# Performance work log

Measured on AMD Instinct MI355X. Metric: run time of the kernel, lower is better.

Reference implementation:

```python
import jax, jax.numpy as jnp
import numpy as np

NUM_HEADS, NUM_KV_HEADS, HEAD_DIM, HIDDEN = 8, 1, 256, 2048
B, S = 1, 4096

def setup_inputs() -> dict:
    key = jax.random.key(0)
    ks = jax.random.split(key, 6)
    sd = 1.0 / np.sqrt(HIDDEN)
    x = jax.random.normal(ks[0], (B, S, HIDDEN), dtype=jnp.float32)
    wq = jax.random.normal(ks[1], (HIDDEN, NUM_HEADS, HEAD_DIM), dtype=jnp.float32) * sd
    bq = jnp.zeros((NUM_HEADS, HEAD_DIM), dtype=jnp.float32)
    wkv = jax.random.normal(ks[2], (HIDDEN, NUM_KV_HEADS, HEAD_DIM), dtype=jnp.float32) * sd
    bkv = jnp.zeros((NUM_KV_HEADS, HEAD_DIM), dtype=jnp.float32)
    wo = jax.random.normal(ks[3], (NUM_HEADS, HEAD_DIM, HIDDEN), dtype=jnp.float32) / np.sqrt(NUM_HEADS * HEAD_DIM)
    bo = jnp.zeros((HIDDEN,), dtype=jnp.float32)
    # causal mask, broadcastable to [b, h, q, k]
    mask = jnp.tril(jnp.ones((S, S), dtype=bool))[None, None, :, :]
    return {"x": x, "wq": wq, "bq": bq, "wkv": wkv, "bkv": bkv, "wo": wo, "bo": bo, "mask": mask}

def reference(x, wq, bq, wkv, bkv, wo, bo, mask):
    # q: [b,s,h,d]; kv: [b,s,kvh,d] -- used as BOTH k and v (as in source)
    q = jnp.einsum('bsh,hnd->bsnd', x, wq) + bq
    kv = jnp.einsum('bsh,hnd->bsnd', x, wkv) + bkv
    q = jnp.transpose(q, (0, 2, 1, 3))   # [b,h,s,d]
    k = jnp.transpose(kv, (0, 2, 1, 3))  # [b,kvh,s,d]
    v = k
    rep = NUM_HEADS // NUM_KV_HEADS
    k = jnp.repeat(k, rep, axis=1)
    v = jnp.repeat(v, rep, axis=1)
    scale = 1.0 / jnp.sqrt(jnp.float32(HEAD_DIM))
    attn = jnp.einsum('bhqd,bhkd->bhqk', q, k) * scale
    attn = jnp.where(mask, attn, -1e9)
    attn = jax.nn.softmax(attn, axis=-1)
    out = jnp.einsum('bhqk,bhkd->bhqd', attn, v)
    out = jnp.transpose(out, (0, 2, 1, 3))  # [b,s,h,d]
    return jnp.einsum('bsnd,ndh->bsh', out, wo) + bo
```

## Files before the change

kernel.cpp:

```cpp
#include <hip/hip_runtime.h>
#include <hip/hip_bf16.h>
#include <stdint.h>

#define HIDDEN 2048
#define SEQ 4096
#define NH 8
#define HD 256

typedef float f32x4 __attribute__((ext_vector_type(4)));
typedef short s16x8 __attribute__((ext_vector_type(8)));
typedef float f32x4v __attribute__((ext_vector_type(4)));

__device__ inline uint16_t f2bf(float f) {
  union { float f; uint32_t u; } v;
  v.f = f;
  uint32_t r = (v.u + 0x7fffu + ((v.u >> 16) & 1u)) >> 16;
  return (uint16_t)r;
}

__device__ inline void gll16(const uint16_t* src, uint16_t* lds) {
  __builtin_amdgcn_global_load_lds(
      (const __attribute__((address_space(1))) unsigned int*)src,
      (__attribute__((address_space(3))) unsigned int*)lds, 16, 0, 0);
}

__global__ __launch_bounds__(256) void cast_kernel(const float* __restrict__ in,
                                                   uint16_t* __restrict__ out, int n4) {
  int i = blockIdx.x * 256 + threadIdx.x;
  if (i >= n4) return;
  f32x4v v = ((const f32x4v*)in)[i];
  union { uint16_t u[4]; uint64_t l; } o;
  o.u[0] = f2bf(v.x); o.u[1] = f2bf(v.y); o.u[2] = f2bf(v.z); o.u[3] = f2bf(v.w);
  ((uint64_t*)out)[i] = o.l;
}

__global__ __launch_bounds__(256) void transpose_cast_kernel(const float* __restrict__ in,
                                                             uint16_t* __restrict__ out,
                                                             int R, int C) {
  __shared__ uint16_t tile[64][65];
  int t = threadIdx.x;
  int ctiles = C >> 6;
  int c0 = (blockIdx.x % ctiles) << 6;
  int r0 = (blockIdx.x / ctiles) << 6;
#pragma unroll
  for (int p = 0; p < 16; ++p) {
    int r = p * 4 + (t >> 6), c = t & 63;
    tile[c][r] = f2bf(in[(size_t)(r0 + r) * C + c0 + c]);
  }
  __syncthreads();
#pragma unroll
  for (int p = 0; p < 16; ++p) {
    int r = p * 4 + (t >> 6), c = t & 63;
    out[(size_t)(c0 + r) * R + r0 + c] = tile[r][c];
  }
}

__device__ inline void gemm_tile_core(const uint16_t* __restrict__ A,
                                      const uint16_t* __restrict__ BT, int K, int m0,
                                      uint16_t* Alds, uint16_t* Blds, f32x4 acc[4][4]) {
  const int t = threadIdx.x, lane = t & 63, wid = t >> 6;
  const int l15 = lane & 15, l4 = lane >> 4;
  const int wm = wid >> 1, wn = wid & 1;
#pragma unroll
  for (int i = 0; i < 4; ++i)
#pragma unroll
    for (int j = 0; j < 4; ++j) acc[i][j] = f32x4{0.f, 0.f, 0.f, 0.f};
  for (int kt = 0; kt < K; kt += 32) {
    __syncthreads();
#pragma unroll
    for (int i = 0; i < 2; ++i) {
      int j = i * 256 + t;
      gll16(A + (size_t)(m0 + (j >> 2)) * K + kt + (j & 3) * 8,
            Alds + (i * 256 + wid * 64) * 8);
    }
#pragma unroll
    for (int i = 0; i < 2; ++i) {
      int j = i * 256 + t;
      gll16(BT + (size_t)(j >> 2) * K + kt + (j & 3) * 8,
            Blds + (i * 256 + wid * 64) * 8);
    }
    __syncthreads();
    s16x8 av[4], bv[4];
#pragma unroll
    for (int mi = 0; mi < 4; ++mi)
      av[mi] = *(const s16x8*)(Alds + (wm * 64 + mi * 16 + l15) * 32 + l4 * 8);
#pragma unroll
    for (int nj = 0; nj < 4; ++nj)
      bv[nj] = *(const s16x8*)(Blds + (wn * 64 + nj * 16 + l15) * 32 + l4 * 8);
#pragma unroll
    for (int mi = 0; mi < 4; ++mi)
#pragma unroll
      for (int nj = 0; nj < 4; ++nj)
        acc[mi][nj] = __builtin_amdgcn_mfma_f32_16x16x32_bf16(av[mi], bv[nj],
                                                              acc[mi][nj], 0, 0, 0);
  }
}

__global__ __launch_bounds__(256) void gemm_qkv_kernel(
    const uint16_t* __restrict__ xb, const uint16_t* __restrict__ wqT,
    const uint16_t* __restrict__ wkvT, const float* __restrict__ bq,
    const float* __restrict__ bkv, uint16_t* __restrict__ Qws,
    uint16_t* __restrict__ Kws, uint16_t* __restrict__ VTws) {
  __shared__ uint16_t Alds[128 * 32], Blds[128 * 32];
  int bid = blockIdx.x;
  int bn = bid % 18, bm = bid / 18;
  int m0 = bm * 128;
  const uint16_t* BT = (bn < 16) ? (wqT + (size_t)bn * 128 * HIDDEN)
                                 : (wkvT + (size_t)(bn - 16) * 128 * HIDDEN);
  f32x4 acc[4][4];
  gemm_tile_core(xb, BT, HIDDEN, m0, Alds, Blds, acc);
  const int lane = threadIdx.x & 63, wid = threadIdx.x >> 6;
  const int l15 = lane & 15, l4 = lane >> 4;
  const int wm = wid >> 1, wn = wid & 1;
#pragma unroll
  for (int mi = 0; mi < 4; ++mi) {
#pragma unroll
    for (int nj = 0; nj < 4; ++nj) {
      int nloc = bn * 128 + wn * 64 + nj * 16 + l15;
#pragma unroll
      for (int r = 0; r < 4; ++r) {
        int m = m0 + wm * 64 + mi * 16 + 4 * l4 + r;
        float v = acc[mi][nj][r];
        if (bn < 16) {
          v += bq[nloc];
          uint16_t b = f2bf(v);
          int head = nloc >> 8, d = nloc & 255;
          Qws[((size_t)head * SEQ + m) * HD + d] = b;
        } else {
          int d = nloc - 2048;
          v += bkv[d];
          uint16_t b = f2bf(v);
          Kws[(size_t)m * HD + d] = b;
          VTws[(size_t)d * SEQ + m] = b;
        }
      }
    }
  }
}

__global__ __launch_bounds__(256) void attn_kernel(const uint16_t* __restrict__ Qws,
                                                   const uint16_t* __restrict__ Kws,
                                                   const uint16_t* __restrict__ VTws,
                                                   uint16_t* __restrict__ Ows) {
  __shared__ unsigned char smem[74752];
  uint16_t* Klds = (uint16_t*)smem;
  uint16_t* VTlds = (uint16_t*)(smem + 32768);
  const int t = threadIdx.x, lane = t & 63, wid = t >> 6;
  const int l15 = lane & 15, l4 = lane >> 4;
  const int bid = blockIdx.x;
  const int head = bid & 7, qb = 63 - (bid >> 3);
  const int qrow = qb * 64 + wid * 16 + l15;
  uint16_t* Pw = (uint16_t*)(smem + 65536 + wid * 2304);

  s16x8 qf[8];
  const uint16_t* qbase = Qws + ((size_t)head * SEQ + qrow) * HD;
#pragma unroll
  for (int kk = 0; kk < 8; ++kk) qf[kk] = *(const s16x8*)(qbase + kk * 32 + l4 * 8);

  float mrun = -INFINITY, lrun = 0.f;
  f32x4 oacc[16];
#pragma unroll
  for (int i = 0; i < 16; ++i) oacc[i] = f32x4{0.f, 0.f, 0.f, 0.f};

  const float sc = 0.09016844005556021f;

  for (int kb = 0; kb <= qb; ++kb) {
    __syncthreads();
#pragma unroll
    for (int i = 0; i < 8; ++i) {
      int j = i * 256 + t;
      int r = j >> 5, cp = j & 31;
      int c = (cp & ~7) | ((cp ^ r) & 7);
      gll16(Kws + (size_t)(kb * 64 + r) * HD + c * 8, Klds + (i * 256 + wid * 64) * 8);
    }
#pragma unroll
    for (int i = 0; i < 8; ++i) {
      int j = i * 256 + t;
      int d = j >> 3, cp = j & 7;
      int c = (cp ^ d) & 7;
      gll16(VTws + (size_t)d * SEQ + kb * 64 + c * 8, VTlds + (i * 256 + wid * 64) * 8);
    }
    __syncthreads();

    f32x4 sacc[4];
#pragma unroll
    for (int i = 0; i < 4; ++i) sacc[i] = f32x4{0.f, 0.f, 0.f, 0.f};
#pragma unroll
    for (int kvt = 0; kvt < 4; ++kvt) {
#pragma unroll
      for (int kk = 0; kk < 8; ++kk) {
        int r = kvt * 16 + l15;
        int c = kk * 4 + l4;
        int cs = (c & ~7) | ((c ^ r) & 7);
        s16x8 kf = *(const s16x8*)(Klds + r * 256 + cs * 8);
        sacc[kvt] = __builtin_amdgcn_mfma_f32_16x16x32_bf16(kf, qf[kk], sacc[kvt], 0, 0, 0);
      }
    }

    float pv[16];
    float vmax = -INFINITY;
#pragma unroll
    for (int kvt = 0; kvt < 4; ++kvt) {
#pragma unroll
      for (int r = 0; r < 4; ++r) {
        float s = sacc[kvt][r] * sc;
        int kv = kb * 64 + kvt * 16 + 4 * l4 + r;
        if (kb == qb && kv > qrow) s = -1e30f;
        pv[kvt * 4 + r] = s;
        vmax = fmaxf(vmax, s);
      }
    }
    vmax = fmaxf(vmax, __shfl_xor(vmax, 16));
    vmax = fmaxf(vmax, __shfl_xor(vmax, 32));
    float mnew = fmaxf(mrun, vmax);
    float alpha = exp2f(mrun - mnew);
    float rsum = 0.f;
#pragma unroll
    for (int i = 0; i < 16; ++i) {
      float p = exp2f(pv[i] - mnew);
      pv[i] = p;
      rsum += p;
    }
    rsum += __shfl_xor(rsum, 16);
    rsum += __shfl_xor(rsum, 32);
    lrun = lrun * alpha + rsum;
    mrun = mnew;
    float a4[4];
#pragma unroll
    for (int r = 0; r < 4; ++r) a4[r] = __shfl(alpha, 4 * l4 + r);
#pragma unroll
    for (int dt = 0; dt < 16; ++dt) {
#pragma unroll
      for (int r = 0; r < 4; ++r) oacc[dt][r] *= a4[r];
    }
#pragma unroll
    for (int kvt = 0; kvt < 4; ++kvt) {
      uint64_t pk = (uint64_t)f2bf(pv[kvt * 4 + 0]) |
                    ((uint64_t)f2bf(pv[kvt * 4 + 1]) << 16) |
                    ((uint64_t)f2bf(pv[kvt * 4 + 2]) << 32) |
                    ((uint64_t)f2bf(pv[kvt * 4 + 3]) << 48);
      *(uint64_t*)(Pw + l15 * 72 + kvt * 16 + l4 * 4) = pk;
    }
#pragma unroll
    for (int kk = 0; kk < 2; ++kk) {
      s16x8 pa = *(const s16x8*)(Pw + l15 * 72 + kk * 32 + l4 * 8);
#pragma unroll
      for (int dt = 0; dt < 16; ++dt) {
        int d = dt * 16 + l15;
        int c = (kk * 4 + l4) ^ (d & 7);
        s16x8 vf = *(const s16x8*)(VTlds + d * 64 + c * 8);
        oacc[dt] = __builtin_amdgcn_mfma_f32_16x16x32_bf16(pa, vf, oacc[dt], 0, 0, 0);
      }
    }
  }

  float linv = 1.0f / lrun;
  float li4[4];
#pragma unroll
  for (int r = 0; r < 4; ++r) li4[r] = __shfl(linv, 4 * l4 + r);
#pragma unroll
  for (int dt = 0; dt < 16; ++dt) {
#pragma unroll
    for (int r = 0; r < 4; ++r) {
      int s = qb * 64 + wid * 16 + 4 * l4 + r;
      int col = head * HD + dt * 16 + l15;
      Ows[(size_t)s * HIDDEN + col] = f2bf(oacc[dt][r] * li4[r]);
    }
  }
}

__global__ __launch_bounds__(256) void gemm_out_kernel(const uint16_t* __restrict__ Ows,
                                                       const uint16_t* __restrict__ woT,
                                                       const float* __restrict__ bo,
                                                       float* __restrict__ Y) {
  __shared__ uint16_t Alds[128 * 32], Blds[128 * 32];
  int bid = blockIdx.x;
  int bn = bid % 16, bm = bid / 16;
  int m0 = bm * 128;
  f32x4 acc[4][4];
  gemm_tile_core(Ows, woT + (size_t)bn * 128 * HIDDEN, HIDDEN, m0, Alds, Blds, acc);
  const int lane = threadIdx.x & 63, wid = threadIdx.x >> 6;
  const int l15 = lane & 15, l4 = lane >> 4;
  const int wm = wid >> 1, wn = wid & 1;
#pragma unroll
  for (int mi = 0; mi < 4; ++mi) {
#pragma unroll
    for (int nj = 0; nj < 4; ++nj) {
      int n = bn * 128 + wn * 64 + nj * 16 + l15;
      float bias = bo[n];
#pragma unroll
      for (int r = 0; r < 4; ++r) {
        int m = m0 + wm * 64 + mi * 16 + 4 * l4 + r;
        Y[(size_t)m * HIDDEN + n] = acc[mi][nj][r] + bias;
      }
    }
  }
}

extern "C" void kernel_launch(void* const* d_in, const int* in_sizes, int n_in,
                              void* d_out, int out_size, void* d_ws, size_t ws_size,
                              hipStream_t stream) {
  const float* x = (const float*)d_in[0];
  const float* wq = (const float*)d_in[1];
  const float* bq = (const float*)d_in[2];
  const float* wkv = (const float*)d_in[3];
  const float* bkv = (const float*)d_in[4];
  const float* wo = (const float*)d_in[5];
  const float* bo = (const float*)d_in[6];
  float* Y = (float*)d_out;

  uint8_t* ws = (uint8_t*)d_ws;
  uint16_t* xb   = (uint16_t*)(ws + 0);
  uint16_t* wqT  = (uint16_t*)(ws + 16777216);
  uint16_t* wkvT = (uint16_t*)(ws + 25165824);
  uint16_t* woT  = (uint16_t*)(ws + 26214400);
  uint16_t* Qws  = (uint16_t*)(ws + 34603008);
  uint16_t* Kws  = (uint16_t*)(ws + 51380224);
  uint16_t* VTws = (uint16_t*)(ws + 53477376);
  uint16_t* Ows  = (uint16_t*)(ws + 55574528);

  cast_kernel<<<8192, 256, 0, stream>>>(x, xb, (SEQ * HIDDEN) / 4);
  transpose_cast_kernel<<<1024, 256, 0, stream>>>(wq, wqT, HIDDEN, 2048);
  transpose_cast_kernel<<<128, 256, 0, stream>>>(wkv, wkvT, HIDDEN, 256);
  transpose_cast_kernel<<<1024, 256, 0, stream>>>(wo, woT, 2048, HIDDEN);
  gemm_qkv_kernel<<<32 * 18, 256, 0, stream>>>(xb, wqT, wkvT, bq, bkv, Qws, Kws, VTws);
  attn_kernel<<<512, 256, 0, stream>>>(Qws, Kws, VTws, Ows);
  gemm_out_kernel<<<32 * 16, 256, 0, stream>>>(Ows, woT, bo, Y);
}
```

Baseline: 461.6 us.

## Double-buffer GEMM and attention loads, pair causal blocks, fold scale into Q

The GEMM core and the attention KV loop now double-buffer their LDS tiles, so the next tile's global-to-LDS load is issued before computing on the current one. Attention pairs a long and a short causal query block in each workgroup (256 blocks instead of 512) to balance work. It also skips the running-max rescale of the output accumulators while the max grows by at most 8, and the softmax scale is folded into Q in the projection epilogue. Both GEMM kernels remap block IDs across XCDs for L2 locality. The larger LDS footprint (about 137KB for attention) limits occupancy to one block per CU.

```diff
diff --git a/kernel.cpp b/kernel.cpp
--- a/kernel.cpp
+++ b/kernel.cpp
@@ -10,6 +10,8 @@
 typedef float f32x4 __attribute__((ext_vector_type(4)));
 typedef short s16x8 __attribute__((ext_vector_type(8)));
 typedef float f32x4v __attribute__((ext_vector_type(4)));
+
+#define QSCALE 0.09016844005556021f
 
 __device__ inline uint16_t f2bf(float f) {
   union { float f; uint32_t u; } v;
@@ -65,28 +67,34 @@
   for (int i = 0; i < 4; ++i)
 #pragma unroll
     for (int j = 0; j < 4; ++j) acc[i][j] = f32x4{0.f, 0.f, 0.f, 0.f};
-  for (int kt = 0; kt < K; kt += 32) {
-    __syncthreads();
+
+  auto stage = [&](int kt, int b) {
 #pragma unroll
     for (int i = 0; i < 2; ++i) {
       int j = i * 256 + t;
       gll16(A + (size_t)(m0 + (j >> 2)) * K + kt + (j & 3) * 8,
-            Alds + (i * 256 + wid * 64) * 8);
+            Alds + b * 4096 + (i * 256 + wid * 64) * 8);
     }
 #pragma unroll
     for (int i = 0; i < 2; ++i) {
       int j = i * 256 + t;
       gll16(BT + (size_t)(j >> 2) * K + kt + (j & 3) * 8,
-            Blds + (i * 256 + wid * 64) * 8);
-    }
+            Blds + b * 4096 + (i * 256 + wid * 64) * 8);
+    }
+  };
+
+  stage(0, 0);
+  int b = 0;
+  for (int kt = 0; kt < K; kt += 32, b ^= 1) {
     __syncthreads();
+    if (kt + 32 < K) stage(kt + 32, b ^ 1);
     s16x8 av[4], bv[4];
 #pragma unroll
     for (int mi = 0; mi < 4; ++mi)
-      av[mi] = *(const s16x8*)(Alds + (wm * 64 + mi * 16 + l15) * 32 + l4 * 8);
+      av[mi] = *(const s16x8*)(Alds + b * 4096 + (wm * 64 + mi * 16 + l15) * 32 + l4 * 8);
 #pragma unroll
     for (int nj = 0; nj < 4; ++nj)
-      bv[nj] = *(const s16x8*)(Blds + (wn * 64 + nj * 16 + l15) * 32 + l4 * 8);
+      bv[nj] = *(const s16x8*)(Blds + b * 4096 + (wn * 64 + nj * 16 + l15) * 32 + l4 * 8);
 #pragma unroll
     for (int mi = 0; mi < 4; ++mi)
 #pragma unroll
@@ -101,8 +109,9 @@
     const uint16_t* __restrict__ wkvT, const float* __restrict__ bq,
     const float* __restrict__ bkv, uint16_t* __restrict__ Qws,
     uint16_t* __restrict__ Kws, uint16_t* __restrict__ VTws) {
-  __shared__ uint16_t Alds[128 * 32], Blds[128 * 32];
-  int bid = blockIdx.x;
+  __shared__ uint16_t Alds[8192], Blds[8192];
+  int b0 = blockIdx.x;
+  int bid = (b0 & 7) * 72 + (b0 >> 3);
   int bn = bid % 18, bm = bid / 18;
   int m0 = bm * 128;
   const uint16_t* BT = (bn < 16) ? (wqT + (size_t)bn * 128 * HIDDEN)
@@ -122,7 +131,7 @@
         int m = m0 + wm * 64 + mi * 16 + 4 * l4 + r;
         float v = acc[mi][nj][r];
         if (bn < 16) {
-          v += bq[nloc];
+          v = (v + bq[nloc]) * QSCALE;
           uint16_t b = f2bf(v);
           int head = nloc >> 8, d = nloc & 255;
           Qws[((size_t)head * SEQ + m) * HD + d] = b;
@@ -142,30 +151,14 @@
                                                    const uint16_t* __restrict__ Kws,
                                                    const uint16_t* __restrict__ VTws,
                                                    uint16_t* __restrict__ Ows) {
-  __shared__ unsigned char smem[74752];
-  uint16_t* Klds = (uint16_t*)smem;
-  uint16_t* VTlds = (uint16_t*)(smem + 32768);
+  __shared__ unsigned char smem[140288];
   const int t = threadIdx.x, lane = t & 63, wid = t >> 6;
   const int l15 = lane & 15, l4 = lane >> 4;
-  const int bid = blockIdx.x;
-  const int head = bid & 7, qb = 63 - (bid >> 3);
-  const int qrow = qb * 64 + wid * 16 + l15;
-  uint16_t* Pw = (uint16_t*)(smem + 65536 + wid * 2304);
-
-  s16x8 qf[8];
-  const uint16_t* qbase = Qws + ((size_t)head * SEQ + qrow) * HD;
-#pragma unroll
-  for (int kk = 0; kk < 8; ++kk) qf[kk] = *(const s16x8*)(qbase + kk * 32 + l4 * 8);
-
-  float mrun = -INFINITY, lrun = 0.f;
-  f32x4 oacc[16];
-#pragma unroll
-  for (int i = 0; i < 16; ++i) oacc[i] = f32x4{0.f, 0.f, 0.f, 0.f};
-
-  const float sc = 0.09016844005556021f;
-
-  for (int kb = 0; kb <= qb; ++kb) {
-    __syncthreads();
+  const int h = blockIdx.x & 7, p = blockIdx.x >> 3;
+  uint16_t* Pw = (uint16_t*)(smem + 131072 + wid * 2304);
+
+  auto stageKV = [&](int kb, int buf) {
+    uint16_t* Klds = (uint16_t*)(smem + buf * 32768);
 #pragma unroll
     for (int i = 0; i < 8; ++i) {
       int j = i * 256 + t;
@@ -173,6 +166,7 @@
       int c = (cp & ~7) | ((cp ^ r) & 7);
       gll16(Kws + (size_t)(kb * 64 + r) * HD + c * 8, Klds + (i * 256 + wid * 64) * 8);
     }
+    uint16_t* VTlds = (uint16_t*)(smem + 65536 + buf * 32768);
 #pragma unroll
     for (int i = 0; i < 8; ++i) {
       int j = i * 256 + t;
@@ -180,91 +174,125 @@
       int c = (cp ^ d) & 7;
       gll16(VTws + (size_t)d * SEQ + kb * 64 + c * 8, VTlds + (i * 256 + wid * 64) * 8);
     }
+  };
+
+  for (int half = 0; half < 2; ++half) {
+    const int qb = half ? p : 63 - p;
+    const int qrow = qb * 64 + wid * 16 + l15;
+
+    s16x8 qf[8];
+    const uint16_t* qbase = Qws + ((size_t)h * SEQ + qrow) * HD;
+#pragma unroll
+    for (int kk = 0; kk < 8; ++kk) qf[kk] = *(const s16x8*)(qbase + kk * 32 + l4 * 8);
+
+    float mrun = -1e30f, lrun = 0.f;
+    f32x4 oacc[16];
+#pragma unroll
+    for (int i = 0; i < 16; ++i) oacc[i] = f32x4{0.f, 0.f, 0.f, 0.f};
+
+    const int nt = qb + 1;
     __syncthreads();
-
-    f32x4 sacc[4];
-#pragma unroll
-    for (int i = 0; i < 4; ++i) sacc[i] = f32x4{0.f, 0.f, 0.f, 0.f};
-#pragma unroll
-    for (int kvt = 0; kvt < 4; ++kvt) {
-#pragma unroll
-      for (int kk = 0; kk < 8; ++kk) {
-        int r = kvt * 16 + l15;
-        int c = kk * 4 + l4;
-        int cs = (c & ~7) | ((c ^ r) & 7);
-        s16x8 kf = *(const s16x8*)(Klds + r * 256 + cs * 8);
-        sacc[kvt] = __builtin_amdgcn_mfma_f32_16x16x32_bf16(kf, qf[kk], sacc[kvt], 0, 0, 0);
-      }
-    }
-
-    float pv[16];
-    float vmax = -INFINITY;
-#pragma unroll
-    for (int kvt = 0; kvt < 4; ++kvt) {
+    stageKV(0, 0);
+
+    for (int kb = 0; kb < nt; ++kb) {
+      const int buf = kb & 1;
+      __syncthreads();
+      if (kb + 1 < nt) stageKV(kb + 1, buf ^ 1);
+      uint16_t* Klds = (uint16_t*)(smem + buf * 32768);
+      uint16_t* VTlds = (uint16_t*)(smem + 65536 + buf * 32768);
+
+      f32x4 sacc[4];
+#pragma unroll
+      for (int i = 0; i < 4; ++i) sacc[i] = f32x4{0.f, 0.f, 0.f, 0.f};
+#pragma unroll
+      for (int kvt = 0; kvt < 4; ++kvt) {
+#pragma unroll
+        for (int kk = 0; kk < 8; ++kk) {
+          int r = kvt * 16 + l15;
+          int c = kk * 4 + l4;
+          int cs = (c & ~7) | ((c ^ r) & 7);
+          s16x8 kf = *(const s16x8*)(Klds + r * 256 + cs * 8);
+          sacc[kvt] = __builtin_amdgcn_mfma_f32_16x16x32_bf16(kf, qf[kk], sacc[kvt], 0, 0, 0);
+        }
+      }
+
+      float pv[16];
+      float vmax = -1e30f;
+      const bool diag = (kb == qb);
+#pragma unroll
+      for (int kvt = 0; kvt < 4; ++kvt) {
+#pragma unroll
+        for (int r = 0; r < 4; ++r) {
+          float s = sacc[kvt][r];
+          if (diag) {
+            int kv = kb * 64 + kvt * 16 + 4 * l4 + r;
+            if (kv > qrow) s = -1e30f;
+          }
+          pv[kvt * 4 + r] = s;
+          vmax = fmaxf(vmax, s);
+        }
+      }
+      vmax = fmaxf(vmax, __shfl_xor(vmax, 16));
+      vmax = fmaxf(vmax, __shfl_xor(vmax, 32));
+
+      if (!__all(vmax - mrun <= 8.0f)) {
+        float mnew = fmaxf(mrun, vmax);
+        float alpha = exp2f(mrun - mnew);
+        float a4[4];
+#pragma unroll
+        for (int r = 0; r < 4; ++r) a4[r] = __shfl(alpha, 4 * l4 + r);
+#pragma unroll
+        for (int dt = 0; dt < 16; ++dt) {
+#pragma unroll
+          for (int r = 0; r < 4; ++r) oacc[dt][r] *= a4[r];
+        }
+        lrun *= alpha;
+        mrun = mnew;
+      }
+      float rsum = 0.f;
+#pragma unroll
+      for (int i = 0; i < 16; ++i) {
+        float pe = exp2f(pv[i] - mrun);
+        pv[i] = pe;
+        rsum += pe;
+      }
+      rsum += __shfl_xor(rsum, 16);
+      rsum += __shfl_xor(rsum, 32);
+      lrun += rsum;
+
+#pragma unroll
+      for (int kvt = 0; kvt < 4; ++kvt) {
+        uint64_t pk = (uint64_t)f2bf(pv[kvt * 4 + 0]) |
+                      ((uint64_t)f2bf(pv[kvt * 4 + 1]) << 16) |
+                      ((uint64_t)f2bf(pv[kvt * 4 + 2]) << 32) |
+                      ((uint64_t)f2bf(pv[kvt * 4 + 3]) << 48);
+        *(uint64_t*)(Pw + l15 * 72 + kvt * 16 + l4 * 4) = pk;
+      }
+#pragma unroll
+      for (int kk = 0; kk < 2; ++kk) {
+        s16x8 pa = *(const s16x8*)(Pw + l15 * 72 + kk * 32 + l4 * 8);
+#pragma unroll
+        for (int dt = 0; dt < 16; ++dt) {
+          int d = dt * 16 + l15;
+          int c = (kk * 4 + l4) ^ (d & 7);
+          s16x8 vf = *(const s16x8*)(VTlds + d * 64 + c * 8);
+          oacc[dt] = __builtin_amdgcn_mfma_f32_16x16x32_bf16(pa, vf, oacc[dt], 0, 0, 0);
+        }
+      }
+    }
+
+    float linv = 1.0f / lrun;
+    float li4[4];
+#pragma unroll
+    for (int r = 0; r < 4; ++r) li4[r] = __shfl(linv, 4 * l4 + r);
+#pragma unroll
+    for (int dt = 0; dt < 16; ++dt) {
 #pragma unroll
       for (int r = 0; r < 4; ++r) {
-        float s = sacc[kvt][r] * sc;
-        int kv = kb * 64 + kvt * 16 + 4 * l4 + r;
-        if (kb == qb && kv > qrow) s = -1e30f;
-        pv[kvt * 4 + r] = s;
-        vmax = fmaxf(vmax, s);
-      }
-    }
-    vmax = fmaxf(vmax, __shfl_xor(vmax, 16));
-    vmax = fmaxf(vmax, __shfl_xor(vmax, 32));
-    float mnew = fmaxf(mrun, vmax);
-    float alpha = exp2f(mrun - mnew);
-    float rsum = 0.f;
-#pragma unroll
-    for (int i = 0; i < 16; ++i) {
-      float p = exp2f(pv[i] - mnew);
-      pv[i] = p;
-      rsum += p;
-    }
-    rsum += __shfl_xor(rsum, 16);
-    rsum += __shfl_xor(rsum, 32);
-    lrun = lrun * alpha + rsum;
-    mrun = mnew;
-    float a4[4];
-#pragma unroll
-    for (int r = 0; r < 4; ++r) a4[r] = __shfl(alpha, 4 * l4 + r);
-#pragma unroll
-    for (int dt = 0; dt < 16; ++dt) {
-#pragma unroll
-      for (int r = 0; r < 4; ++r) oacc[dt][r] *= a4[r];
-    }
-#pragma unroll
-    for (int kvt = 0; kvt < 4; ++kvt) {
-      uint64_t pk = (uint64_t)f2bf(pv[kvt * 4 + 0]) |
-                    ((uint64_t)f2bf(pv[kvt * 4 + 1]) << 16) |
-                    ((uint64_t)f2bf(pv[kvt * 4 + 2]) << 32) |
-                    ((uint64_t)f2bf(pv[kvt * 4 + 3]) << 48);
-      *(uint64_t*)(Pw + l15 * 72 + kvt * 16 + l4 * 4) = pk;
-    }
-#pragma unroll
-    for (int kk = 0; kk < 2; ++kk) {
-      s16x8 pa = *(const s16x8*)(Pw + l15 * 72 + kk * 32 + l4 * 8);
-#pragma unroll
-      for (int dt = 0; dt < 16; ++dt) {
-        int d = dt * 16 + l15;
-        int c = (kk * 4 + l4) ^ (d & 7);
-        s16x8 vf = *(const s16x8*)(VTlds + d * 64 + c * 8);
-        oacc[dt] = __builtin_amdgcn_mfma_f32_16x16x32_bf16(pa, vf, oacc[dt], 0, 0, 0);
-      }
-    }
-  }
-
-  float linv = 1.0f / lrun;
-  float li4[4];
-#pragma unroll
-  for (int r = 0; r < 4; ++r) li4[r] = __shfl(linv, 4 * l4 + r);
-#pragma unroll
-  for (int dt = 0; dt < 16; ++dt) {
-#pragma unroll
-    for (int r = 0; r < 4; ++r) {
-      int s = qb * 64 + wid * 16 + 4 * l4 + r;
-      int col = head * HD + dt * 16 + l15;
-      Ows[(size_t)s * HIDDEN + col] = f2bf(oacc[dt][r] * li4[r]);
+        int s = qb * 64 + wid * 16 + 4 * l4 + r;
+        int col = h * HD + dt * 16 + l15;
+        Ows[(size_t)s * HIDDEN + col] = f2bf(oacc[dt][r] * li4[r]);
+      }
     }
   }
 }
@@ -273,8 +301,9 @@
                                                        const uint16_t* __restrict__ woT,
                                                        const float* __restrict__ bo,
                                                        float* __restrict__ Y) {
-  __shared__ uint16_t Alds[128 * 32], Blds[128 * 32];
-  int bid = blockIdx.x;
+  __shared__ uint16_t Alds[8192], Blds[8192];
+  int b0 = blockIdx.x;
+  int bid = (b0 & 7) * 64 + (b0 >> 3);
   int bn = bid % 16, bm = bid / 16;
   int m0 = bm * 128;
   f32x4 acc[4][4];
@@ -324,6 +353,6 @@
   transpose_cast_kernel<<<128, 256, 0, stream>>>(wkv, wkvT, HIDDEN, 256);
   transpose_cast_kernel<<<1024, 256, 0, stream>>>(wo, woT, 2048, HIDDEN);
   gemm_qkv_kernel<<<32 * 18, 256, 0, stream>>>(xb, wqT, wkvT, bq, bkv, Qws, Kws, VTws);
-  attn_kernel<<<512, 256, 0, stream>>>(Qws, Kws, VTws, Ows);
+  attn_kernel<<<256, 256, 0, stream>>>(Qws, Kws, VTws, Ows);
   gemm_out_kernel<<<32 * 16, 256, 0, stream>>>(Ows, woT, bo, Y);
 }
```

Measured after the change: 442.5 us. 1.04x faster.
